# Kernel optimization log

Hardware: AMD Instinct MI355X
Metric: run time of the kernel (lower is better)

Reference implementation:

```python
import jax, jax.numpy as jnp
import numpy as np

EMB = 256
HEADS = 4
HEAD_DIM = EMB // HEADS
N = 4096
M = 4096


def setup_inputs() -> dict:
    key = jax.random.key(0)
    ks = jax.random.split(key, 7)
    s = 1.0 / np.sqrt(EMB)  # keep logits in a sane range
    return {
        "A": jax.random.normal(ks[0], (N, EMB), jnp.float32),
        "B": jax.random.normal(ks[1], (M, EMB), jnp.float32),
        "Wq": jax.random.normal(ks[2], (EMB, EMB), jnp.float32) * s,
        "Wk": jax.random.normal(ks[3], (EMB, EMB), jnp.float32) * s,
        "Wv": jax.random.normal(ks[4], (EMB, EMB), jnp.float32) * s,
        "Wo": jax.random.normal(ks[5], (EMB, EMB), jnp.float32) * s,
        "bo": jnp.zeros((EMB,), jnp.float32),
    }


def _cross_attend(X, Y, Wq, Wk, Wv, Wo, bo):
    # X attends to Y. X:[n,emb], Y:[m,emb]
    scale = jnp.asarray(np.sqrt(HEAD_DIM), X.dtype)
    Q = (X @ Wq.T).reshape(X.shape[0], HEADS, HEAD_DIM)  # [n,h,d]
    K = (Y @ Wk.T).reshape(Y.shape[0], HEADS, HEAD_DIM)  # [m,h,d]
    V = (Y @ Wv.T).reshape(Y.shape[0], HEADS, HEAD_DIM)  # [m,h,d]
    scores = jnp.einsum("nhd,mhd->hnm", Q, K) / scale      # [h,n,m]
    attn = jax.nn.softmax(scores, axis=-1)                   # dropout p=0.0 -> identity
    ctx = jnp.einsum("hnm,mhd->nhd", attn, V).reshape(X.shape[0], EMB)
    return ctx @ Wo.T + bo + X                               # out proj + residual


def reference(A, B, Wq, Wk, Wv, Wo, bo):
    A_out = _cross_attend(A, B, Wq, Wk, Wv, Wo, bo)
    B_out = _cross_attend(B, A, Wq, Wk, Wv, Wo, bo)
    return (A_out, B_out)
```

## Files before the change

### kernel.cpp

```cpp
#include <hip/hip_runtime.h>
#include <hip/hip_bf16.h>
#include <math.h>

#define EMB 256
#define HEADS 4
#define HD 64
#define NTOK 4096

typedef __attribute__((ext_vector_type(8))) short bf16x8;
typedef __attribute__((ext_vector_type(4))) float f32x4;
typedef __attribute__((ext_vector_type(16))) float f32x16;

#define MFMA16(a, b, c) __builtin_amdgcn_mfma_f32_16x16x32_bf16(a, b, c, 0, 0, 0)
#define MFMA32(a, b, c) __builtin_amdgcn_mfma_f32_32x32x16_bf16(a, b, c, 0, 0, 0)

static __device__ __forceinline__ ushort f2bf(float f) {
    __hip_bfloat16 h = __float2bfloat16(f);
    return *(ushort*)&h;
}
static __device__ __forceinline__ float ex2(float x) { return __builtin_amdgcn_exp2f(x); }
static __device__ __forceinline__ uint pkbf(float lo, float hi) {
    uint r;
    asm("v_cvt_pk_bf16_f32 %0, %1, %2" : "=v"(r) : "v"(lo), "v"(hi));
    return r;
}
static __device__ __forceinline__ float max3f(float a, float b, float c) {
    float r;
    asm("v_max3_f32 %0, %1, %2, %3" : "=v"(r) : "v"(a), "v"(b), "v"(c));
    return r;
}
static __device__ __forceinline__ bf16x8 cvt8(float4 a, float4 b) {
    union { uint u[4]; bf16x8 h; } pk;
    pk.u[0] = pkbf(a.x, a.y);
    pk.u[1] = pkbf(a.z, a.w);
    pk.u[2] = pkbf(b.x, b.y);
    pk.u[3] = pkbf(b.z, b.w);
    return pk.h;
}
static __device__ __forceinline__ float bf2f(ushort u) {
    return __uint_as_float(((uint)u) << 16);
}

__global__ void cvtW(const float* __restrict__ Wq, const float* __restrict__ Wk,
                     const float* __restrict__ Wv, const float* __restrict__ Wo,
                     ushort* __restrict__ Wall) {
    const float* s = (blockIdx.y == 0) ? Wq : (blockIdx.y == 1) ? Wk : (blockIdx.y == 2) ? Wv : Wo;
    ushort* d = Wall + (size_t)blockIdx.y * 65536;
    int i = (blockIdx.x * 256 + threadIdx.x) * 4;
    float4 v = *(const float4*)(s + i);
    ushort4 o;
    o.x = f2bf(v.x); o.y = f2bf(v.y); o.z = f2bf(v.z); o.w = f2bf(v.w);
    *(ushort4*)(d + i) = o;
}

__global__ __launch_bounds__(256) void qkv_proj(const float* __restrict__ Xa,
                                                const float* __restrict__ Xb,
                                                const ushort* __restrict__ Wall,
                                                ushort* __restrict__ Q0, ushort* __restrict__ K1, ushort* __restrict__ Vt1,
                                                ushort* __restrict__ Q1, ushort* __restrict__ K0, ushort* __restrict__ Vt0) {
    int w = threadIdx.x >> 6, lane = threadIdx.x & 63;
    int lr = lane & 15, lg = lane >> 4;
    int z = blockIdx.z;
    int kind = (z < 3) ? z : z - 3;
    const float* X = (z < 3) ? Xa : Xb;
    ushort* Qo = (z < 3) ? Q0 : Q1;
    ushort* Ko = (z < 3) ? K1 : K0;
    ushort* Vto = (z < 3) ? Vt1 : Vt0;
    const ushort* W = Wall + (size_t)kind * 65536;
    int rbase = blockIdx.x * 64 + w * 16;
    int cbase = blockIdx.y * 64;

    f32x4 acc[4] = {};
#pragma unroll
    for (int kk = 0; kk < 256; kk += 32) {
        const float* xr = X + (size_t)(rbase + lr) * EMB + kk + lg * 8;
        bf16x8 a = cvt8(*(const float4*)xr, *(const float4*)(xr + 4));
#pragma unroll
        for (int cj = 0; cj < 4; ++cj) {
            bf16x8 b = *(const bf16x8*)(W + (size_t)(cbase + cj * 16 + lr) * EMB + kk + lg * 8);
            acc[cj] = MFMA16(a, b, acc[cj]);
        }
    }
    const float QS = 0.125f * 1.4426950408889634f;
#pragma unroll
    for (int cj = 0; cj < 4; ++cj)
#pragma unroll
        for (int j = 0; j < 4; ++j) {
            int R = rbase + lg * 4 + j;
            int col = cbase + cj * 16 + lr;
            float v = acc[cj][j];
            if (kind == 0) {
                Qo[(size_t)R * EMB + col] = f2bf(v * QS);
            } else if (kind == 1) {
                Ko[(size_t)R * EMB + col] = f2bf(v);
            } else {
                int h = col >> 6, d = col & 63;
                int Rp = (R & ~12) | ((R & 4) << 1) | ((R & 8) >> 1);
                Vto[(size_t)h * HD * NTOK + (size_t)d * NTOK + Rp] = f2bf(v);
            }
        }
}

__global__ __launch_bounds__(256, 4) void attn(const ushort* __restrict__ Q0,
                                               const ushort* __restrict__ K0,
                                               const ushort* __restrict__ Vt0,
                                               const ushort* __restrict__ Q1,
                                               const ushort* __restrict__ K1,
                                               const ushort* __restrict__ Vt1,
                                               ushort* __restrict__ Opart,
                                               float* __restrict__ ML) {
    __shared__ ushort lK[2][64 * 64];
    __shared__ ushort lV[2][64 * 64];

    int fb = blockIdx.x + 32 * blockIdx.y + 128 * blockIdx.z;
    int nf = (fb & 7) * 128 + (fb >> 3);
    int qt = nf & 31;
    int head = (nf >> 5) & 3;
    int z = nf >> 7;
    int dir = z >> 2, split = z & 3;
    int kv0 = split * 1024;

    const ushort* Q = dir ? Q1 : Q0;
    const ushort* K = dir ? K1 : K0;
    const ushort* Vt = dir ? Vt1 : Vt0;
    const ushort* Vth = Vt + (size_t)head * HD * NTOK;

    int wq = threadIdx.x >> 6;
    int lane = threadIdx.x & 63;
    int l31 = lane & 31, hi = lane >> 5;

    int qg = qt * 128 + wq * 32 + l31;
    bf16x8 qf[4];
#pragma unroll
    for (int ks = 0; ks < 4; ++ks)
        qf[ks] = *(const bf16x8*)(Q + (size_t)qg * EMB + head * 64 + ks * 16 + hi * 8);

    int srow = threadIdx.x >> 3, sseg = threadIdx.x & 7;
    int ssw0 = (sseg ^ (srow & 7)) * 8;
    int ssw1 = (sseg ^ ((srow + 32) & 7)) * 8;

    uint4 rk0 = *(const uint4*)(K + (size_t)(kv0 + srow) * EMB + head * 64 + sseg * 8);
    uint4 rk1 = *(const uint4*)(K + (size_t)(kv0 + srow + 32) * EMB + head * 64 + sseg * 8);
    uint4 rv0 = *(const uint4*)(Vth + (size_t)srow * NTOK + kv0 + sseg * 8);
    uint4 rv1 = *(const uint4*)(Vth + (size_t)(srow + 32) * NTOK + kv0 + sseg * 8);

    float m = -1e30f, ls = 0.0f;
    f32x16 oacc0 = {};
    f32x16 oacc1 = {};
    int sw = l31 & 7;

    for (int t = 0; t < 16; ++t) {
        int cur = t & 1;
        ushort* lk = &lK[cur][0];
        ushort* lv = &lV[cur][0];
        *(uint4*)(&lk[srow * 64 + ssw0]) = rk0;
        *(uint4*)(&lk[(srow + 32) * 64 + ssw1]) = rk1;
        *(uint4*)(&lv[srow * 64 + ssw0]) = rv0;
        *(uint4*)(&lv[(srow + 32) * 64 + ssw1]) = rv1;
        __syncthreads();

        if (t < 15) {
            int nkv = kv0 + (t + 1) * 64;
            rk0 = *(const uint4*)(K + (size_t)(nkv + srow) * EMB + head * 64 + sseg * 8);
            rk1 = *(const uint4*)(K + (size_t)(nkv + srow + 32) * EMB + head * 64 + sseg * 8);
            rv0 = *(const uint4*)(Vth + (size_t)srow * NTOK + nkv + sseg * 8);
            rv1 = *(const uint4*)(Vth + (size_t)(srow + 32) * NTOK + nkv + sseg * 8);
        }

        f32x16 sA = {}, sB = {};
        __builtin_amdgcn_s_setprio(1);
#pragma unroll
        for (int ks = 0; ks < 4; ++ks) {
            bf16x8 ka = *(const bf16x8*)(&lk[l31 * 64 + ((ks * 2 + hi) ^ sw) * 8]);
            bf16x8 kb = *(const bf16x8*)(&lk[(32 + l31) * 64 + ((ks * 2 + hi) ^ sw) * 8]);
            sA = MFMA32(ka, qf[ks], sA);
            sB = MFMA32(kb, qf[ks], sB);
        }
        __builtin_amdgcn_s_setprio(0);

        float t0 = max3f(sA[0], sA[1], sA[2]);
        float t1 = max3f(sA[3], sA[4], sA[5]);
        float t2 = max3f(sA[6], sA[7], sA[8]);
        float t3 = max3f(sA[9], sA[10], sA[11]);
        float t4 = max3f(sA[12], sA[13], sA[14]);
        float t5 = max3f(sB[0], sB[1], sB[2]);
        float t6 = max3f(sB[3], sB[4], sB[5]);
        float t7 = max3f(sB[6], sB[7], sB[8]);
        float t8 = max3f(sB[9], sB[10], sB[11]);
        float t9 = max3f(sB[12], sB[13], sB[14]);
        float ta = fmaxf(sA[15], sB[15]);
        float u0 = max3f(t0, t1, t2);
        float u1 = max3f(t3, t4, t5);
        float u2 = max3f(t6, t7, t8);
        float u3 = fmaxf(t9, ta);
        float tmax = fmaxf(max3f(u0, u1, u2), u3);
        tmax = fmaxf(tmax, __shfl_xor(tmax, 32));

        if (__any(tmax > m + 8.0f)) {
            float mn = fmaxf(m, tmax);
            float sc = ex2(m - mn);
            m = mn;
            ls *= sc;
#pragma unroll
            for (int r = 0; r < 16; ++r) { oacc0[r] *= sc; oacc1[r] *= sc; }
        }

#pragma unroll
        for (int r = 0; r < 16; ++r) sA[r] = ex2(sA[r] - m);
#pragma unroll
        for (int r = 0; r < 16; ++r) sB[r] = ex2(sB[r] - m);

        float s1[16];
#pragma unroll
        for (int i = 0; i < 8; ++i) s1[i] = sA[2 * i] + sA[2 * i + 1];
#pragma unroll
        for (int i = 0; i < 8; ++i) s1[8 + i] = sB[2 * i] + sB[2 * i + 1];
#pragma unroll
        for (int w2 = 8; w2 >= 1; w2 >>= 1)
#pragma unroll
            for (int i = 0; i < 8; ++i)
                if (i < w2) s1[i] = s1[2 * i] + s1[2 * i + 1];
        float rs = s1[0];
        rs += __shfl_xor(rs, 32);
        ls += rs;

        bf16x8 pa[4];
#pragma unroll
        for (int ks = 0; ks < 4; ++ks) {
            union { uint u[4]; bf16x8 h; } pk;
#pragma unroll
            for (int j = 0; j < 4; ++j) {
                float lo = (ks < 2) ? sA[(ks & 1) * 8 + 2 * j] : sB[(ks & 1) * 8 + 2 * j];
                float hv = (ks < 2) ? sA[(ks & 1) * 8 + 2 * j + 1] : sB[(ks & 1) * 8 + 2 * j + 1];
                pk.u[j] = pkbf(lo, hv);
            }
            pa[ks] = pk.h;
        }

        __builtin_amdgcn_s_setprio(1);
#pragma unroll
        for (int ks = 0; ks < 4; ++ks) {
            bf16x8 va = *(const bf16x8*)(&lv[l31 * 64 + ((ks * 2 + hi) ^ sw) * 8]);
            bf16x8 vb = *(const bf16x8*)(&lv[(32 + l31) * 64 + ((ks * 2 + hi) ^ sw) * 8]);
            oacc0 = MFMA32(va, pa[ks], oacc0);
            oacc1 = MFMA32(vb, pa[ks], oacc1);
        }
        __builtin_amdgcn_s_setprio(0);
    }

    ushort* Ob = Opart + ((size_t)z * 4096 + qg) * 256 + head * 64;
#pragma unroll
    for (int r = 0; r < 16; ++r) {
        int crow = (r & 3) + 8 * (r >> 2) + 4 * hi;
        Ob[crow] = f2bf(oacc0[r]);
        Ob[32 + crow] = f2bf(oacc1[r]);
    }
    if (hi == 0) {
        float2* mlp = (float2*)ML;
        mlp[((size_t)z * 4 + head) * 4096 + qg] = make_float2(m, ls);
    }
}

__global__ __launch_bounds__(256) void out_proj(const ushort* __restrict__ Opart,
                                                const float* __restrict__ ML,
                                                const ushort* __restrict__ Wo,
                                                const float* __restrict__ bo,
                                                const float* __restrict__ A,
                                                const float* __restrict__ B,
                                                float* __restrict__ out) {
    int dir = blockIdx.z;
    const float* X = dir ? B : A;
    float* o = out + (size_t)dir * NTOK * EMB;

    int w = threadIdx.x >> 6, lane = threadIdx.x & 63;
    int lr = lane & 15, lg = lane >> 4;
    int rbase = blockIdx.x * 64 + w * 16;
    int cbase = blockIdx.y * 64;
    int R = rbase + lr;

    const float2* mlp = (const float2*)ML;
    float Wm[4][4];
#pragma unroll
    for (int h = 0; h < 4; ++h) {
        float2 ml[4];
        float M = -1e30f;
#pragma unroll
        for (int s = 0; s < 4; ++s) {
            ml[s] = mlp[((size_t)(dir * 4 + s) * 4 + h) * 4096 + R];
            M = fmaxf(M, ml[s].x);
        }
        float denom = 0.0f, a[4];
#pragma unroll
        for (int s = 0; s < 4; ++s) { a[s] = ex2(ml[s].x - M); denom += a[s] * ml[s].y; }
        float inv = 1.0f / denom;
#pragma unroll
        for (int s = 0; s < 4; ++s) Wm[h][s] = a[s] * inv;
    }

    const ushort* Or[4];
#pragma unroll
    for (int s = 0; s < 4; ++s)
        Or[s] = Opart + ((size_t)(dir * 4 + s) * 4096 + R) * 256;

    f32x4 acc[4] = {};
#pragma unroll
    for (int kk = 0; kk < 256; kk += 32) {
        int h = kk >> 6;
        bf16x8 xs0 = *(const bf16x8*)(Or[0] + kk + lg * 8);
        bf16x8 xs1 = *(const bf16x8*)(Or[1] + kk + lg * 8);
        bf16x8 xs2 = *(const bf16x8*)(Or[2] + kk + lg * 8);
        bf16x8 xs3 = *(const bf16x8*)(Or[3] + kk + lg * 8);
        float cv[8];
#pragma unroll
        for (int u = 0; u < 8; ++u) {
            cv[u] = Wm[h][0] * bf2f((ushort)xs0[u]) + Wm[h][1] * bf2f((ushort)xs1[u])
                  + Wm[h][2] * bf2f((ushort)xs2[u]) + Wm[h][3] * bf2f((ushort)xs3[u]);
        }
        float4 c0 = {cv[0], cv[1], cv[2], cv[3]};
        float4 c1 = {cv[4], cv[5], cv[6], cv[7]};
        bf16x8 a = cvt8(c0, c1);
#pragma unroll
        for (int cj = 0; cj < 4; ++cj) {
            bf16x8 b = *(const bf16x8*)(Wo + (size_t)(cbase + cj * 16 + lr) * EMB + kk + lg * 8);
            acc[cj] = MFMA16(a, b, acc[cj]);
        }
    }
#pragma unroll
    for (int cj = 0; cj < 4; ++cj)
#pragma unroll
        for (int j = 0; j < 4; ++j) {
            int Rr = rbase + lg * 4 + j;
            int col = cbase + cj * 16 + lr;
            o[(size_t)Rr * EMB + col] = acc[cj][j] + bo[col] + X[(size_t)Rr * EMB + col];
        }
}

extern "C" void kernel_launch(void* const* d_in, const int* in_sizes, int n_in,
                              void* d_out, int out_size, void* d_ws, size_t ws_size,
                              hipStream_t stream) {
    const float* A  = (const float*)d_in[0];
    const float* B  = (const float*)d_in[1];
    const float* Wq = (const float*)d_in[2];
    const float* Wk = (const float*)d_in[3];
    const float* Wv = (const float*)d_in[4];
    const float* Wo = (const float*)d_in[5];
    const float* bo = (const float*)d_in[6];
    float* out = (float*)d_out;

    ushort* ws = (ushort*)d_ws;
    const size_t TE = (size_t)NTOK * EMB;
    ushort* wall = ws;
    ushort* q0  = wall + 4 * 65536;
    ushort* q1  = q0 + TE;
    ushort* k0  = q1 + TE;
    ushort* k1  = k0 + TE;
    ushort* vt0 = k1 + TE;
    ushort* vt1 = vt0 + TE;
    ushort* Opart = vt1 + TE;
    float* ML = (float*)(Opart + (size_t)8 * 4096 * 256);

    cvtW<<<dim3(64, 4), 256, 0, stream>>>(Wq, Wk, Wv, Wo, wall);

    qkv_proj<<<dim3(64, 4, 6), 256, 0, stream>>>(A, B, wall, q0, k1, vt1, q1, k0, vt0);

    attn<<<dim3(32, 4, 8), 256, 0, stream>>>(q0, k0, vt0, q1, k1, vt1, Opart, ML);

    out_proj<<<dim3(64, 4, 2), 256, 0, stream>>>(Opart, ML, wall + 3 * 65536, bo, A, B, out);
}
```

Baseline: 113.8 us.

## Fuse QKV projections per block, double KV splits, single-buffer LDS, add merge kernel

qkv_proj now computes Q, K and V in one block, reusing each converted activation tile across all three weight matrices instead of reloading X per projection. Attention doubles the KV split count to 8 with half the tiles each and drops LDS double buffering in favour of an extra barrier, with launch bounds raised to allow 8 blocks per CU for more occupancy. The split-softmax combine moves into a separate merge kernel that writes a bf16 context, so out_proj becomes a plain GEMM. The cost is twice the partial-output traffic, an extra launch, and exposed load latency from the single LDS buffer.

Result: slower. 373.4 us (+228.2%).

```diff
diff --git a/kernel.cpp b/kernel.cpp
--- a/kernel.cpp
+++ b/kernel.cpp
@@ -61,24 +61,26 @@
     int w = threadIdx.x >> 6, lane = threadIdx.x & 63;
     int lr = lane & 15, lg = lane >> 4;
     int z = blockIdx.z;
-    int kind = (z < 3) ? z : z - 3;
-    const float* X = (z < 3) ? Xa : Xb;
-    ushort* Qo = (z < 3) ? Q0 : Q1;
-    ushort* Ko = (z < 3) ? K1 : K0;
-    ushort* Vto = (z < 3) ? Vt1 : Vt0;
-    const ushort* W = Wall + (size_t)kind * 65536;
+    const float* X = z ? Xb : Xa;
+    ushort* Qo = z ? Q1 : Q0;
+    ushort* Ko = z ? K0 : K1;
+    ushort* Vto = z ? Vt0 : Vt1;
     int rbase = blockIdx.x * 64 + w * 16;
     int cbase = blockIdx.y * 64;
 
-    f32x4 acc[4] = {};
+    f32x4 acc[3][4] = {};
 #pragma unroll
     for (int kk = 0; kk < 256; kk += 32) {
         const float* xr = X + (size_t)(rbase + lr) * EMB + kk + lg * 8;
         bf16x8 a = cvt8(*(const float4*)xr, *(const float4*)(xr + 4));
 #pragma unroll
-        for (int cj = 0; cj < 4; ++cj) {
-            bf16x8 b = *(const bf16x8*)(W + (size_t)(cbase + cj * 16 + lr) * EMB + kk + lg * 8);
-            acc[cj] = MFMA16(a, b, acc[cj]);
+        for (int kind = 0; kind < 3; ++kind) {
+            const ushort* W = Wall + (size_t)kind * 65536;
+#pragma unroll
+            for (int cj = 0; cj < 4; ++cj) {
+                bf16x8 b = *(const bf16x8*)(W + (size_t)(cbase + cj * 16 + lr) * EMB + kk + lg * 8);
+                acc[kind][cj] = MFMA16(a, b, acc[kind][cj]);
+            }
         }
     }
     const float QS = 0.125f * 1.4426950408889634f;
@@ -88,20 +90,15 @@
         for (int j = 0; j < 4; ++j) {
             int R = rbase + lg * 4 + j;
             int col = cbase + cj * 16 + lr;
-            float v = acc[cj][j];
-            if (kind == 0) {
-                Qo[(size_t)R * EMB + col] = f2bf(v * QS);
-            } else if (kind == 1) {
-                Ko[(size_t)R * EMB + col] = f2bf(v);
-            } else {
-                int h = col >> 6, d = col & 63;
-                int Rp = (R & ~12) | ((R & 4) << 1) | ((R & 8) >> 1);
-                Vto[(size_t)h * HD * NTOK + (size_t)d * NTOK + Rp] = f2bf(v);
-            }
-        }
-}
-
-__global__ __launch_bounds__(256, 4) void attn(const ushort* __restrict__ Q0,
+            Qo[(size_t)R * EMB + col] = f2bf(acc[0][cj][j] * QS);
+            Ko[(size_t)R * EMB + col] = f2bf(acc[1][cj][j]);
+            int h = col >> 6, d = col & 63;
+            int Rp = (R & ~12) | ((R & 4) << 1) | ((R & 8) >> 1);
+            Vto[(size_t)h * HD * NTOK + (size_t)d * NTOK + Rp] = f2bf(acc[2][cj][j]);
+        }
+}
+
+__global__ __launch_bounds__(256, 8) void attn(const ushort* __restrict__ Q0,
                                                const ushort* __restrict__ K0,
                                                const ushort* __restrict__ Vt0,
                                                const ushort* __restrict__ Q1,
@@ -109,16 +106,16 @@
                                                const ushort* __restrict__ Vt1,
                                                ushort* __restrict__ Opart,
                                                float* __restrict__ ML) {
-    __shared__ ushort lK[2][64 * 64];
-    __shared__ ushort lV[2][64 * 64];
+    __shared__ ushort lK[64 * 64];
+    __shared__ ushort lV[64 * 64];
 
     int fb = blockIdx.x + 32 * blockIdx.y + 128 * blockIdx.z;
-    int nf = (fb & 7) * 128 + (fb >> 3);
+    int nf = (fb & 7) * 256 + (fb >> 3);
     int qt = nf & 31;
     int head = (nf >> 5) & 3;
     int z = nf >> 7;
-    int dir = z >> 2, split = z & 3;
-    int kv0 = split * 1024;
+    int dir = z >> 3, split = z & 7;
+    int kv0 = split * 512;
 
     const ushort* Q = dir ? Q1 : Q0;
     const ushort* K = dir ? K1 : K0;
@@ -136,8 +133,7 @@
         qf[ks] = *(const bf16x8*)(Q + (size_t)qg * EMB + head * 64 + ks * 16 + hi * 8);
 
     int srow = threadIdx.x >> 3, sseg = threadIdx.x & 7;
-    int ssw0 = (sseg ^ (srow & 7)) * 8;
-    int ssw1 = (sseg ^ ((srow + 32) & 7)) * 8;
+    int ssw = (sseg ^ ((srow >> 2) & 7)) * 8;
 
     uint4 rk0 = *(const uint4*)(K + (size_t)(kv0 + srow) * EMB + head * 64 + sseg * 8);
     uint4 rk1 = *(const uint4*)(K + (size_t)(kv0 + srow + 32) * EMB + head * 64 + sseg * 8);
@@ -147,19 +143,17 @@
     float m = -1e30f, ls = 0.0f;
     f32x16 oacc0 = {};
     f32x16 oacc1 = {};
-    int sw = l31 & 7;
-
-    for (int t = 0; t < 16; ++t) {
-        int cur = t & 1;
-        ushort* lk = &lK[cur][0];
-        ushort* lv = &lV[cur][0];
-        *(uint4*)(&lk[srow * 64 + ssw0]) = rk0;
-        *(uint4*)(&lk[(srow + 32) * 64 + ssw1]) = rk1;
-        *(uint4*)(&lv[srow * 64 + ssw0]) = rv0;
-        *(uint4*)(&lv[(srow + 32) * 64 + ssw1]) = rv1;
+    int sw = (l31 >> 2) & 7;
+
+    for (int t = 0; t < 8; ++t) {
+        if (t) __syncthreads();
+        *(uint4*)(&lK[srow * 64 + ssw]) = rk0;
+        *(uint4*)(&lK[(srow + 32) * 64 + ssw]) = rk1;
+        *(uint4*)(&lV[srow * 64 + ssw]) = rv0;
+        *(uint4*)(&lV[(srow + 32) * 64 + ssw]) = rv1;
         __syncthreads();
 
-        if (t < 15) {
+        if (t < 7) {
             int nkv = kv0 + (t + 1) * 64;
             rk0 = *(const uint4*)(K + (size_t)(nkv + srow) * EMB + head * 64 + sseg * 8);
             rk1 = *(const uint4*)(K + (size_t)(nkv + srow + 32) * EMB + head * 64 + sseg * 8);
@@ -171,8 +165,8 @@
         __builtin_amdgcn_s_setprio(1);
 #pragma unroll
         for (int ks = 0; ks < 4; ++ks) {
-            bf16x8 ka = *(const bf16x8*)(&lk[l31 * 64 + ((ks * 2 + hi) ^ sw) * 8]);
-            bf16x8 kb = *(const bf16x8*)(&lk[(32 + l31) * 64 + ((ks * 2 + hi) ^ sw) * 8]);
+            bf16x8 ka = *(const bf16x8*)(&lK[l31 * 64 + ((ks * 2 + hi) ^ sw) * 8]);
+            bf16x8 kb = *(const bf16x8*)(&lK[(32 + l31) * 64 + ((ks * 2 + hi) ^ sw) * 8]);
             sA = MFMA32(ka, qf[ks], sA);
             sB = MFMA32(kb, qf[ks], sB);
         }
@@ -240,8 +234,8 @@
         __builtin_amdgcn_s_setprio(1);
 #pragma unroll
         for (int ks = 0; ks < 4; ++ks) {
-            bf16x8 va = *(const bf16x8*)(&lv[l31 * 64 + ((ks * 2 + hi) ^ sw) * 8]);
-            bf16x8 vb = *(const bf16x8*)(&lv[(32 + l31) * 64 + ((ks * 2 + hi) ^ sw) * 8]);
+            bf16x8 va = *(const bf16x8*)(&lV[l31 * 64 + ((ks * 2 + hi) ^ sw) * 8]);
+            bf16x8 vb = *(const bf16x8*)(&lV[(32 + l31) * 64 + ((ks * 2 + hi) ^ sw) * 8]);
             oacc0 = MFMA32(va, pa[ks], oacc0);
             oacc1 = MFMA32(vb, pa[ks], oacc1);
         }
@@ -261,14 +255,52 @@
     }
 }
 
-__global__ __launch_bounds__(256) void out_proj(const ushort* __restrict__ Opart,
-                                                const float* __restrict__ ML,
+__global__ __launch_bounds__(256) void merge(const ushort* __restrict__ Opart,
+                                             const float* __restrict__ ML,
+                                             ushort* __restrict__ C0,
+                                             ushort* __restrict__ C1) {
+    int idx = blockIdx.x * 256 + threadIdx.x;
+    int dblk = idx & 7;
+    int head = (idx >> 3) & 3;
+    int q = (idx >> 5) & 4095;
+    int dir = idx >> 17;
+
+    const float2* mlp = (const float2*)ML;
+    float2 ml[8];
+    float M = -1e30f;
+#pragma unroll
+    for (int s = 0; s < 8; ++s) {
+        ml[s] = mlp[((size_t)(dir * 8 + s) * 4 + head) * 4096 + q];
+        M = fmaxf(M, ml[s].x);
+    }
+    float denom = 0.0f, a[8];
+#pragma unroll
+    for (int s = 0; s < 8; ++s) { a[s] = ex2(ml[s].x - M); denom += a[s] * ml[s].y; }
+    float inv = 1.0f / denom;
+
+    float accv[8] = {};
+#pragma unroll
+    for (int s = 0; s < 8; ++s) {
+        float ws = a[s] * inv;
+        bf16x8 x = *(const bf16x8*)(Opart + ((size_t)(dir * 8 + s) * 4096 + q) * 256 + head * 64 + dblk * 8);
+#pragma unroll
+        for (int u = 0; u < 8; ++u) accv[u] += ws * bf2f((ushort)x[u]);
+    }
+    float4 c0 = {accv[0], accv[1], accv[2], accv[3]};
+    float4 c1 = {accv[4], accv[5], accv[6], accv[7]};
+    ushort* C = (dir ? C1 : C0) + (size_t)q * 256 + head * 64 + dblk * 8;
+    *(bf16x8*)C = cvt8(c0, c1);
+}
+
+__global__ __launch_bounds__(256) void out_proj(const ushort* __restrict__ C0,
+                                                const ushort* __restrict__ C1,
                                                 const ushort* __restrict__ Wo,
                                                 const float* __restrict__ bo,
                                                 const float* __restrict__ A,
                                                 const float* __restrict__ B,
                                                 float* __restrict__ out) {
     int dir = blockIdx.z;
+    const ushort* Ctx = dir ? C1 : C0;
     const float* X = dir ? B : A;
     float* o = out + (size_t)dir * NTOK * EMB;
 
@@ -276,49 +308,11 @@
     int lr = lane & 15, lg = lane >> 4;
     int rbase = blockIdx.x * 64 + w * 16;
     int cbase = blockIdx.y * 64;
-    int R = rbase + lr;
-
-    const float2* mlp = (const float2*)ML;
-    float Wm[4][4];
-#pragma unroll
-    for (int h = 0; h < 4; ++h) {
-        float2 ml[4];
-        float M = -1e30f;
-#pragma unroll
-        for (int s = 0; s < 4; ++s) {
-            ml[s] = mlp[((size_t)(dir * 4 + s) * 4 + h) * 4096 + R];
-            M = fmaxf(M, ml[s].x);
-        }
-        float denom = 0.0f, a[4];
-#pragma unroll
-        for (int s = 0; s < 4; ++s) { a[s] = ex2(ml[s].x - M); denom += a[s] * ml[s].y; }
-        float inv = 1.0f / denom;
-#pragma unroll
-        for (int s = 0; s < 4; ++s) Wm[h][s] = a[s] * inv;
-    }
-
-    const ushort* Or[4];
-#pragma unroll
-    for (int s = 0; s < 4; ++s)
-        Or[s] = Opart + ((size_t)(dir * 4 + s) * 4096 + R) * 256;
 
     f32x4 acc[4] = {};
 #pragma unroll
     for (int kk = 0; kk < 256; kk += 32) {
-        int h = kk >> 6;
-        bf16x8 xs0 = *(const bf16x8*)(Or[0] + kk + lg * 8);
-        bf16x8 xs1 = *(const bf16x8*)(Or[1] + kk + lg * 8);
-        bf16x8 xs2 = *(const bf16x8*)(Or[2] + kk + lg * 8);
-        bf16x8 xs3 = *(const bf16x8*)(Or[3] + kk + lg * 8);
-        float cv[8];
-#pragma unroll
-        for (int u = 0; u < 8; ++u) {
-            cv[u] = Wm[h][0] * bf2f((ushort)xs0[u]) + Wm[h][1] * bf2f((ushort)xs1[u])
-                  + Wm[h][2] * bf2f((ushort)xs2[u]) + Wm[h][3] * bf2f((ushort)xs3[u]);
-        }
-        float4 c0 = {cv[0], cv[1], cv[2], cv[3]};
-        float4 c1 = {cv[4], cv[5], cv[6], cv[7]};
-        bf16x8 a = cvt8(c0, c1);
+        bf16x8 a = *(const bf16x8*)(Ctx + (size_t)(rbase + lr) * EMB + kk + lg * 8);
 #pragma unroll
         for (int cj = 0; cj < 4; ++cj) {
             bf16x8 b = *(const bf16x8*)(Wo + (size_t)(cbase + cj * 16 + lr) * EMB + kk + lg * 8);
@@ -329,9 +323,9 @@
     for (int cj = 0; cj < 4; ++cj)
 #pragma unroll
         for (int j = 0; j < 4; ++j) {
-            int Rr = rbase + lg * 4 + j;
+            int R = rbase + lg * 4 + j;
             int col = cbase + cj * 16 + lr;
-            o[(size_t)Rr * EMB + col] = acc[cj][j] + bo[col] + X[(size_t)Rr * EMB + col];
+            o[(size_t)R * EMB + col] = acc[cj][j] + bo[col] + X[(size_t)R * EMB + col];
         }
 }
 
@@ -356,14 +350,18 @@
     ushort* k1  = k0 + TE;
     ushort* vt0 = k1 + TE;
     ushort* vt1 = vt0 + TE;
-    ushort* Opart = vt1 + TE;
-    float* ML = (float*)(Opart + (size_t)8 * 4096 * 256);
+    ushort* c0  = vt1 + TE;
+    ushort* c1  = c0 + TE;
+    ushort* Opart = c1 + TE;
+    float* ML = (float*)(Opart + (size_t)16 * 4096 * 256);
 
     cvtW<<<dim3(64, 4), 256, 0, stream>>>(Wq, Wk, Wv, Wo, wall);
 
-    qkv_proj<<<dim3(64, 4, 6), 256, 0, stream>>>(A, B, wall, q0, k1, vt1, q1, k0, vt0);
-
-    attn<<<dim3(32, 4, 8), 256, 0, stream>>>(q0, k0, vt0, q1, k1, vt1, Opart, ML);
-
-    out_proj<<<dim3(64, 4, 2), 256, 0, stream>>>(Opart, ML, wall + 3 * 65536, bo, A, B, out);
-}
+    qkv_proj<<<dim3(64, 4, 2), 256, 0, stream>>>(A, B, wall, q0, k1, vt1, q1, k0, vt0);
+
+    attn<<<dim3(32, 4, 16), 256, 0, stream>>>(q0, k0, vt0, q1, k1, vt1, Opart, ML);
+
+    merge<<<dim3(1024), 256, 0, stream>>>(Opart, ML, c0, c1);
+
+    out_proj<<<dim3(64, 4, 2), 256, 0, stream>>>(c0, c1, wall + 3 * 65536, bo, A, B, out);
+}
```
